# Optimization experiments

Hardware: AMD Instinct MI355X
Metric: run time of the kernel (lower is better)

The kernel has to match this reference:

```python
import jax, jax.numpy as jnp
import numpy as np
from jax import lax

ACT_BITS = 8
O, C, K = 256, 128, 3
STRIDE, PAD = 1, 1


def setup_inputs() -> dict:
    key = jax.random.key(0)
    kx, kw = jax.random.split(key)
    x = jax.random.uniform(kx, (16, C, 56, 56), dtype=jnp.float32)
    weight = jax.random.normal(kw, (O, C, K, K), dtype=jnp.float32)
    wrange = 2 ** 8  # weight_bits
    qw = jnp.clip(jnp.round(weight * (wrange - 1)), 0, wrange - 1)
    # PCILT: pcilt[o,c,kh,kw,i] = qw[o,c,kh,kw] * i  for i in [0, 2^act_bits)
    A = 2 ** ACT_BITS
    pcilt = qw[..., None] * jnp.arange(A, dtype=jnp.float32)  # [O,C,K,K,A]
    bias = jnp.zeros((O,), dtype=jnp.float32)
    return {"x": x, "pcilt": pcilt, "bias": bias}


def reference(x, pcilt, bias):
    A = pcilt.shape[-1]
    # quantize activations to integer LUT indices in [0, A-1]
    xq = jnp.clip(jnp.round(x * (A - 1)), 0.0, A - 1.0)
    # The gather-and-sum  out[b,o,h,w] = sum_{c,kh,kw} pcilt[o,c,kh,kw, idx]
    # is mathematically identical to a conv with qw = pcilt[...,1] applied to the
    # (float-cast) quantized indices, since pcilt[...,i] == qw * i exactly.
    qw = pcilt[..., 1]  # [O,C,K,K] quantized weights
    out = lax.conv_general_dilated(
        xq, qw,
        window_strides=(STRIDE, STRIDE),
        padding=((PAD, PAD), (PAD, PAD)),
        dimension_numbers=("NCHW", "OIHW", "NCHW"),
    )
    return out + bias[None, :, None, None]
```

## Files before the change

### kernel.cpp

```cpp
#include <hip/hip_runtime.h>
#include <stdint.h>

typedef unsigned short u16;
typedef __bf16 bf16x8 __attribute__((ext_vector_type(8)));
typedef float f32x4 __attribute__((ext_vector_type(4)));

#define B_N   16
#define C_CH  128
#define O_CH  256
#define HW    56
#define PH    58
#define PW    72

#define GLOBAL_AS __attribute__((address_space(1)))
#define LDS_AS    __attribute__((address_space(3)))

__device__ __forceinline__ void glds16(const u16* g, u16* l) {
    __builtin_amdgcn_global_load_lds((const GLOBAL_AS void*)g, (LDS_AS void*)l, 16, 0, 0);
}

__global__ __launch_bounds__(256) void quant_pad(const float* __restrict__ x,
                                                 u16* __restrict__ xp) {
    __shared__ u16 Lt[C_CH][58];
    const int hp = blockIdx.x;
    const int b = blockIdx.y;
    const int tid = threadIdx.x;
    const int h = hp - 1;
    const bool interior = (unsigned)h < HW;

    if (interior) {
        for (int i = 0; i < 28; ++i) {
            int idx = i * 256 + tid;
            int c = idx / HW, w = idx % HW;
            float v = x[((b * C_CH + c) * HW + h) * HW + w];
            float q = fminf(fmaxf(rintf(v * 255.0f), 0.0f), 255.0f);
            Lt[c][w] = (u16)(__float_as_uint(q) >> 16);
        }
    }
    __syncthreads();
    u16* dst = xp + ((size_t)(b * PH + hp) * PW) * C_CH;
    for (int j = 0; j < 36; ++j) {
        int idx = j * 256 + tid;
        int wp = idx / C_CH, c = idx % C_CH;
        int w = wp - 1;
        u16 bits = 0;
        if (interior && (unsigned)w < HW) bits = Lt[c][w];
        dst[idx] = bits;
    }
}

__global__ __launch_bounds__(256) void make_w(const float* __restrict__ pcilt,
                                              u16* __restrict__ Bq) {
    int idx = blockIdx.x * 256 + threadIdx.x;
    int c = idx % C_CH;
    int o = (idx / C_CH) % O_CH;
    int r = idx / (C_CH * O_CH);
    float v = pcilt[(size_t)(((o * C_CH + c) * 9 + r)) * 256 + 1];
    Bq[idx] = (u16)(__float_as_uint(v) >> 16);
}

__global__ __launch_bounds__(256) void conv_mfma(const u16* __restrict__ xp,
                                                 const u16* __restrict__ Bq,
                                                 const float* __restrict__ bias,
                                                 float* __restrict__ out) {
    __shared__ __align__(16) u16 Ws[4][128][8];
    __shared__ __align__(16) u16 Is[4][128][8];

    const int tid = threadIdx.x;
    const int o_blk = blockIdx.x * 128;
    const int h0 = blockIdx.y * 2;
    const int b = blockIdx.z;

    const int lane = tid & 63;
    const int wid = tid >> 6;
    const int wo = wid & 1;
    const int wm = wid >> 1;

    f32x4 acc[4][4];
#pragma unroll
    for (int i = 0; i < 4; i++)
#pragma unroll
        for (int j = 0; j < 4; j++) acc[i][j] = (f32x4){0.f, 0.f, 0.f, 0.f};

    const u16* pI0 = xp + ((size_t)(b * PH + h0) * PW + lane) * C_CH + wid * 8;
    const u16* pI1 = pI0 + (size_t)PW * C_CH;
    const u16* pW0 = Bq + (size_t)(o_blk + lane) * C_CH + wid * 8;
    const u16* pW1 = pW0 + 64 * C_CH;
    u16* lI0 = &Is[wid][0][0];
    u16* lI1 = &Is[wid][64][0];
    u16* lW0 = &Ws[wid][0][0];
    u16* lW1 = &Ws[wid][64][0];

    const int quad = lane >> 4;
    const int lrow = lane & 15;

    for (int r = 0; r < 9; ++r) {
        const int kh = r / 3, kw = r % 3;
        const int offI_r = (kh * PW + kw) * C_CH;
        const int offW_r = r * O_CH * C_CH;
#pragma unroll
        for (int cc = 0; cc < 4; ++cc) {
            const int offI = offI_r + cc * 32;
            const int offW = offW_r + cc * 32;
            __syncthreads();
            glds16(pI0 + offI, lI0);
            glds16(pI1 + offI, lI1);
            glds16(pW0 + offW, lW0);
            glds16(pW1 + offW, lW1);
            __syncthreads();

            bf16x8 af[4], bfr[4];
#pragma unroll
            for (int i = 0; i < 4; i++)
                af[i] = *(const bf16x8*)&Ws[quad][wo * 64 + i * 16 + lrow][0];
#pragma unroll
            for (int j = 0; j < 4; j++)
                bfr[j] = *(const bf16x8*)&Is[quad][wm * 64 + j * 16 + lrow][0];
#pragma unroll
            for (int i = 0; i < 4; i++)
#pragma unroll
                for (int j = 0; j < 4; j++)
                    acc[i][j] = __builtin_amdgcn_mfma_f32_16x16x32_bf16(af[i], bfr[j], acc[i][j], 0, 0, 0);
        }
    }

    const int hh = h0 + wm;
#pragma unroll
    for (int i = 0; i < 4; i++) {
        const int obase = o_blk + wo * 64 + i * 16 + quad * 4;
#pragma unroll
        for (int j = 0; j < 4; j++) {
            const int w = j * 16 + lrow;
            if (w < HW) {
#pragma unroll
                for (int rg = 0; rg < 4; ++rg) {
                    const int o = obase + rg;
                    out[(((size_t)b * O_CH + o) * HW + hh) * HW + w] = acc[i][j][rg] + bias[o];
                }
            }
        }
    }
}

extern "C" void kernel_launch(void* const* d_in, const int* in_sizes, int n_in,
                              void* d_out, int out_size, void* d_ws, size_t ws_size,
                              hipStream_t stream) {
    const float* x     = (const float*)d_in[0];
    const float* pcilt = (const float*)d_in[1];
    const float* bias  = (const float*)d_in[2];
    float* out = (float*)d_out;

    u16* xp = (u16*)d_ws;
    u16* Bq = xp + (size_t)B_N * PH * PW * C_CH;

    quant_pad<<<dim3(PH, B_N), 256, 0, stream>>>(x, xp);
    make_w<<<(9 * O_CH * C_CH) / 256, 256, 0, stream>>>(pcilt, Bq);
    conv_mfma<<<dim3(O_CH / 128, HW / 2, B_N), dim3(256), 0, stream>>>(xp, Bq, bias, out);
}
```

Baseline: 455.4 us.

## Reblock activations and weights into channel-group layout, load weights directly to registers

Activations are stored as [b][h][channel-group of 8][w][8] and weights as [r][cg][o][8], so each MFMA fragment is one contiguous 16-byte load. Weight fragments now go straight from global memory into registers, and the LDS weight staging is removed. Each barrier pair now covers 64 channels instead of 32, which halves the number of synchronizations in the main loop. Quantization also uses float4 loads and vectorized stores. The cost is uncoalesced, latency-exposed global weight loads on every iteration.

```diff
diff --git a/kernel.cpp b/kernel.cpp
--- a/kernel.cpp
+++ b/kernel.cpp
@@ -4,6 +4,8 @@
 typedef unsigned short u16;
 typedef __bf16 bf16x8 __attribute__((ext_vector_type(8)));
 typedef float f32x4 __attribute__((ext_vector_type(4)));
+typedef unsigned short u16x4 __attribute__((ext_vector_type(4)));
+typedef unsigned short u16x8 __attribute__((ext_vector_type(8)));
 
 #define B_N   16
 #define C_CH  128
@@ -11,6 +13,7 @@
 #define HW    56
 #define PH    58
 #define PW    72
+#define NCG   16
 
 #define GLOBAL_AS __attribute__((address_space(1)))
 #define LDS_AS    __attribute__((address_space(3)))
@@ -20,8 +23,8 @@
 }
 
 __global__ __launch_bounds__(256) void quant_pad(const float* __restrict__ x,
-                                                 u16* __restrict__ xp) {
-    __shared__ u16 Lt[C_CH][58];
+                                                 u16* __restrict__ xq) {
+    __shared__ u16 Lt[C_CH][57];
     const int hp = blockIdx.x;
     const int b = blockIdx.y;
     const int tid = threadIdx.x;
@@ -29,42 +32,57 @@
     const bool interior = (unsigned)h < HW;
 
     if (interior) {
-        for (int i = 0; i < 28; ++i) {
-            int idx = i * 256 + tid;
-            int c = idx / HW, w = idx % HW;
-            float v = x[((b * C_CH + c) * HW + h) * HW + w];
-            float q = fminf(fmaxf(rintf(v * 255.0f), 0.0f), 255.0f);
-            Lt[c][w] = (u16)(__float_as_uint(q) >> 16);
+        const float* xr = x + ((size_t)b * C_CH * HW + h) * HW;
+        for (int i = 0; i < 7; ++i) {
+            int u = i * 256 + tid;
+            int c = u / 14, w4 = u % 14;
+            float4 v = *(const float4*)(xr + (size_t)c * (HW * HW) + w4 * 4);
+            float q0 = fminf(fmaxf(rintf(v.x * 255.0f), 0.0f), 255.0f);
+            float q1 = fminf(fmaxf(rintf(v.y * 255.0f), 0.0f), 255.0f);
+            float q2 = fminf(fmaxf(rintf(v.z * 255.0f), 0.0f), 255.0f);
+            float q3 = fminf(fmaxf(rintf(v.w * 255.0f), 0.0f), 255.0f);
+            Lt[c][w4 * 4 + 0] = (u16)(__float_as_uint(q0) >> 16);
+            Lt[c][w4 * 4 + 1] = (u16)(__float_as_uint(q1) >> 16);
+            Lt[c][w4 * 4 + 2] = (u16)(__float_as_uint(q2) >> 16);
+            Lt[c][w4 * 4 + 3] = (u16)(__float_as_uint(q3) >> 16);
         }
     }
     __syncthreads();
-    u16* dst = xp + ((size_t)(b * PH + hp) * PW) * C_CH;
-    for (int j = 0; j < 36; ++j) {
-        int idx = j * 256 + tid;
-        int wp = idx / C_CH, c = idx % C_CH;
+    u16* dst = xq + (size_t)(b * PH + hp) * (NCG * PW * 8);
+    for (int j = 0; j < 9; ++j) {
+        int u = j * 256 + tid;
+        int c8b = (u & 1) * 4;
+        int wp = (u >> 1) % PW;
+        int cg = u / (2 * PW);
         int w = wp - 1;
-        u16 bits = 0;
-        if (interior && (unsigned)w < HW) bits = Lt[c][w];
-        dst[idx] = bits;
+        u16x4 v = (u16x4){0, 0, 0, 0};
+        if (interior && (unsigned)w < HW) {
+#pragma unroll
+            for (int e = 0; e < 4; ++e) v[e] = Lt[cg * 8 + c8b + e][w];
+        }
+        *(u16x4*)(dst + (size_t)u * 4) = v;
     }
 }
 
 __global__ __launch_bounds__(256) void make_w(const float* __restrict__ pcilt,
-                                              u16* __restrict__ Bq) {
-    int idx = blockIdx.x * 256 + threadIdx.x;
-    int c = idx % C_CH;
-    int o = (idx / C_CH) % O_CH;
-    int r = idx / (C_CH * O_CH);
-    float v = pcilt[(size_t)(((o * C_CH + c) * 9 + r)) * 256 + 1];
-    Bq[idx] = (u16)(__float_as_uint(v) >> 16);
+                                              u16* __restrict__ Bw) {
+    int u = blockIdx.x * 256 + threadIdx.x;
+    int o = u & 255;
+    int cg = (u >> 8) & 15;
+    int r = u >> 12;
+    const float* src = pcilt + ((size_t)(o * C_CH + cg * 8) * 9 + r) * 256 + 1;
+    u16x8 v;
+#pragma unroll
+    for (int e = 0; e < 8; ++e)
+        v[e] = (u16)(__float_as_uint(src[(size_t)e * (9 * 256)]) >> 16);
+    *(u16x8*)(Bw + (size_t)u * 8) = v;
 }
 
-__global__ __launch_bounds__(256) void conv_mfma(const u16* __restrict__ xp,
-                                                 const u16* __restrict__ Bq,
+__global__ __launch_bounds__(256) void conv_mfma(const u16* __restrict__ xq,
+                                                 const u16* __restrict__ Bw,
                                                  const float* __restrict__ bias,
                                                  float* __restrict__ out) {
-    __shared__ __align__(16) u16 Ws[4][128][8];
-    __shared__ __align__(16) u16 Is[4][128][8];
+    __shared__ __align__(16) u16 Is[8][128][8];
 
     const int tid = threadIdx.x;
     const int o_blk = blockIdx.x * 128;
@@ -75,6 +93,8 @@
     const int wid = tid >> 6;
     const int wo = wid & 1;
     const int wm = wid >> 1;
+    const int quad = lane >> 4;
+    const int lrow = lane & 15;
 
     f32x4 acc[4][4];
 #pragma unroll
@@ -82,45 +102,46 @@
 #pragma unroll
         for (int j = 0; j < 4; j++) acc[i][j] = (f32x4){0.f, 0.f, 0.f, 0.f};
 
-    const u16* pI0 = xp + ((size_t)(b * PH + h0) * PW + lane) * C_CH + wid * 8;
-    const u16* pI1 = pI0 + (size_t)PW * C_CH;
-    const u16* pW0 = Bq + (size_t)(o_blk + lane) * C_CH + wid * 8;
-    const u16* pW1 = pW0 + 64 * C_CH;
-    u16* lI0 = &Is[wid][0][0];
-    u16* lI1 = &Is[wid][64][0];
-    u16* lW0 = &Ws[wid][0][0];
-    u16* lW1 = &Ws[wid][64][0];
-
-    const int quad = lane >> 4;
-    const int lrow = lane & 15;
+    const u16* wbase = Bw + (size_t)(o_blk + wo * 64 + lrow) * 8;
 
     for (int r = 0; r < 9; ++r) {
         const int kh = r / 3, kw = r % 3;
-        const int offI_r = (kh * PW + kw) * C_CH;
-        const int offW_r = r * O_CH * C_CH;
 #pragma unroll
-        for (int cc = 0; cc < 4; ++cc) {
-            const int offI = offI_r + cc * 32;
-            const int offW = offW_r + cc * 32;
+        for (int half = 0; half < 2; ++half) {
             __syncthreads();
-            glds16(pI0 + offI, lI0);
-            glds16(pI1 + offI, lI1);
-            glds16(pW0 + offW, lW0);
-            glds16(pW1 + offW, lW1);
+#pragma unroll
+            for (int gg = 0; gg < 2; ++gg) {
+                const int g = wid + gg * 4;
+                const int cg = half * 8 + g;
+#pragma unroll
+                for (int dh = 0; dh < 2; ++dh) {
+                    const u16* src = xq +
+                        ((size_t)((b * PH + h0 + dh + kh) * NCG + cg) * PW + kw + lane) * 8;
+                    glds16(src, &Is[g][dh * 64][0]);
+                }
+            }
+            bf16x8 af[2][4];
+#pragma unroll
+            for (int s = 0; s < 2; ++s) {
+                const int cgw = r * 16 + half * 8 + s * 4 + quad;
+#pragma unroll
+                for (int i = 0; i < 4; ++i)
+                    af[s][i] = *(const bf16x8*)(wbase + ((size_t)cgw * 256 + i * 16) * 8);
+            }
             __syncthreads();
-
-            bf16x8 af[4], bfr[4];
+            bf16x8 bfr[2][4];
 #pragma unroll
-            for (int i = 0; i < 4; i++)
-                af[i] = *(const bf16x8*)&Ws[quad][wo * 64 + i * 16 + lrow][0];
+            for (int s = 0; s < 2; ++s)
 #pragma unroll
-            for (int j = 0; j < 4; j++)
-                bfr[j] = *(const bf16x8*)&Is[quad][wm * 64 + j * 16 + lrow][0];
+                for (int j = 0; j < 4; ++j)
+                    bfr[s][j] = *(const bf16x8*)&Is[s * 4 + quad][wm * 64 + j * 16 + lrow][0];
 #pragma unroll
-            for (int i = 0; i < 4; i++)
+            for (int s = 0; s < 2; ++s)
 #pragma unroll
-                for (int j = 0; j < 4; j++)
-                    acc[i][j] = __builtin_amdgcn_mfma_f32_16x16x32_bf16(af[i], bfr[j], acc[i][j], 0, 0, 0);
+                for (int i = 0; i < 4; ++i)
+#pragma unroll
+                    for (int j = 0; j < 4; ++j)
+                        acc[i][j] = __builtin_amdgcn_mfma_f32_16x16x32_bf16(af[s][i], bfr[s][j], acc[i][j], 0, 0, 0);
         }
     }
 
@@ -150,10 +171,10 @@
     const float* bias  = (const float*)d_in[2];
     float* out = (float*)d_out;
 
-    u16* xp = (u16*)d_ws;
-    u16* Bq = xp + (size_t)B_N * PH * PW * C_CH;
+    u16* xq = (u16*)d_ws;
+    u16* Bw = xq + (size_t)B_N * PH * NCG * PW * 8;
 
-    quant_pad<<<dim3(PH, B_N), 256, 0, stream>>>(x, xp);
-    make_w<<<(9 * O_CH * C_CH) / 256, 256, 0, stream>>>(pcilt, Bq);
-    conv_mfma<<<dim3(O_CH / 128, HW / 2, B_N), dim3(256), 0, stream>>>(xp, Bq, bias, out);
+    quant_pad<<<dim3(PH, B_N), 256, 0, stream>>>(x, xq);
+    make_w<<<(9 * NCG * O_CH * 8) / (8 * 256), 256, 0, stream>>>(pcilt, Bw);
+    conv_mfma<<<dim3(O_CH / 128, HW / 2, B_N), dim3(256), 0, stream>>>(xq, Bw, bias, out);
 }
```

Result: faster. 411.1 us (-9.7%).
